# Optimization experiments

Hardware: AMD Instinct MI355X
Metric: run time of the kernel (lower is better)

Reference implementation:

```python
import jax, jax.numpy as jnp
import numpy as np

B, S, H = 4, 512, 1024
E, K, I = 8, 2, 2048

def setup_inputs() -> dict:
    key = jax.random.key(0)
    k1, k2, k3, k4, k5 = jax.random.split(key, 5)
    scale_h = 1.0 / np.sqrt(H)
    scale_i = 1.0 / np.sqrt(I)
    return {
        "hidden_states": jax.random.normal(k1, (B, S, H), dtype=jnp.float32),
        "router_w": jax.random.normal(k2, (E, H), dtype=jnp.float32) * scale_h,
        "w_gate": jax.random.normal(k3, (E, H, I), dtype=jnp.float32) * scale_h,
        "w_up": jax.random.normal(k4, (E, H, I), dtype=jnp.float32) * scale_h,
        "w_down": jax.random.normal(k5, (E, I, H), dtype=jnp.float32) * scale_i,
    }

def reference(hidden_states, router_w, w_gate, w_up, w_down):
    b, s, h = hidden_states.shape
    x = hidden_states.reshape(-1, h)              # [T, H] tokens
    T = x.shape[0]

    # ---- RouterTopK: fp32 linear -> softmax over all experts -> top-k ----
    router_logits = x.astype(jnp.float32) @ router_w.T          # [T, E]
    probs = jax.nn.softmax(router_logits, axis=-1)               # [T, E]
    top_vals, top_idx = jax.lax.top_k(probs, K)                  # [T, K]

    # normalize_top_k_affinities (norm_topk_prob=True)
    top_vals = top_vals / jnp.sum(top_vals, axis=-1, keepdims=True)

    # scatter normalized affinities into a dense [T, E] combine matrix
    aff = jnp.zeros((T, E), dtype=x.dtype).at[jnp.arange(T)[:, None], top_idx].set(top_vals.astype(x.dtype))

    # ---- ExpertMLPs: GLU (swiglu) per expert, combine weighted by affinity ----
    # Dense-per-expert computation; non-selected experts contribute 0 via aff.
    gate = jnp.einsum('th,ehi->eti', x, w_gate)                  # [E, T, I]
    up = jnp.einsum('th,ehi->eti', x, w_up)                      # [E, T, I]
    act = jax.nn.silu(gate) * up                                 # [E, T, I]
    expert_out = jnp.einsum('eti,eih->eth', act, w_down)         # [E, T, H]
    out = jnp.einsum('eth,te->th', expert_out, aff)              # [T, H]

    # _reduce_output: all-reduce over TP/world group -> identity single-device
    return out.reshape(b, s, h)
```

## Files before the change

### kernel.cpp

```cpp
#include <hip/hip_runtime.h>
#include <hip/hip_bf16.h>

#define T_TOK 2048
#define H_DIM 1024
#define E_N   8
#define I_DIM 2048

#define NT_MAX 40
#define MAX_SLOTS 5120

typedef unsigned short u16;
typedef unsigned int   u32;
typedef __bf16 bf16_t;
typedef bf16_t bf16x8 __attribute__((ext_vector_type(8)));
typedef u16    u16x8  __attribute__((ext_vector_type(8)));
typedef float  f32x4  __attribute__((ext_vector_type(4)));

#define MFMA __builtin_amdgcn_mfma_f32_16x16x32_bf16

__device__ __forceinline__ u16 bfbits(float f) {
    bf16_t b = (bf16_t)f;
    return __builtin_bit_cast(u16, b);
}

__device__ __forceinline__ void gload_lds16(const void* g, void* l) {
    __builtin_amdgcn_global_load_lds(
        (const __attribute__((address_space(1))) void*)g,
        (__attribute__((address_space(3))) void*)l, 16, 0, 0);
}

__device__ __forceinline__ int tile_off(int n, int kb) {
    return n * 64 + ((kb ^ ((n >> 1) & 7)) << 3);
}
__device__ __forceinline__ int a_off(int row, int kslot) {
    return row * 64 + ((kslot ^ (row & 7)) << 3);
}

__global__ __launch_bounds__(256) void prep_k(
    const float* __restrict__ x, const float* __restrict__ rw,
    const float* __restrict__ wg, const float* __restrict__ wu, const float* __restrict__ wd,
    u16* __restrict__ tg, u16* __restrict__ tu, u16* __restrict__ td,
    int* __restrict__ cnt, int* __restrict__ tok, float* __restrict__ wts,
    u16* __restrict__ xbf)
{
    __shared__ float S[64][132];
    int bid = blockIdx.x;

    if (bid >= 6144) {
        int wid = threadIdx.x >> 6, lane = threadIdx.x & 63;
        int t = (bid - 6144) * 4 + wid;
        const float* xr = x + (size_t)t * H_DIM;
        u16* xbr = xbf + (size_t)t * H_DIM;
        float acc[E_N];
#pragma unroll
        for (int e = 0; e < E_N; e++) acc[e] = 0.f;
        for (int j = 0; j < H_DIM / 64; j++) {
            float xv = xr[lane + 64 * j];
            xbr[lane + 64 * j] = bfbits(xv);
#pragma unroll
            for (int e = 0; e < E_N; e++)
                acc[e] += xv * rw[e * H_DIM + lane + 64 * j];
        }
#pragma unroll
        for (int e = 0; e < E_N; e++) {
            float v = acc[e];
            for (int off = 32; off; off >>= 1) v += __shfl_xor(v, off);
            acc[e] = v;
        }
        if (lane == 0) {
            int i0 = 0; float m0 = acc[0];
#pragma unroll
            for (int e = 1; e < E_N; e++) if (acc[e] > m0) { m0 = acc[e]; i0 = e; }
            int i1 = -1; float m1 = -INFINITY;
#pragma unroll
            for (int e = 0; e < E_N; e++) if (e != i0 && acc[e] > m1) { m1 = acc[e]; i1 = e; }
            float w0 = 1.f / (1.f + expf(m1 - m0));
            float w1 = 1.f - w0;
            int p0 = atomicAdd(&cnt[i0], 1);
            tok[i0 * T_TOK + p0] = t; wts[i0 * T_TOK + p0] = w0;
            int p1 = atomicAdd(&cnt[i1], 1);
            tok[i1 * T_TOK + p1] = t; wts[i1 * T_TOK + p1] = w1;
        }
        return;
    }

    int kind = bid >> 11;
    int ti = bid & 2047;
    const float* src; u16* dst; int nstr;
    if (kind < 2) {
        const float* w = kind ? wu : wg;
        int e = ti >> 8, b = ti & 15;
        int p = (ti >> 4) & 15;
        src = w + ((size_t)e * H_DIM + b * 64) * I_DIM + p * 128;
        nstr = I_DIM;
        dst = (kind ? tu : tg) + (size_t)ti * 8192;
    } else {
        int e = ti >> 8, r = ti & 255;
        int p = r >> 5, b = r & 31;
        src = wd + ((size_t)e * I_DIM + b * 64) * H_DIM + p * 128;
        nstr = H_DIM;
        dst = td + (size_t)ti * 8192;
    }
    int tid = threadIdx.x;
#pragma unroll
    for (int i = 0; i < 8; i++) {
        int idx = tid + i * 256;
        int k = idx >> 5, c4 = idx & 31;
        float4 v = *reinterpret_cast<const float4*>(src + (size_t)k * nstr + c4 * 4);
        *reinterpret_cast<float4*>(&S[k][c4 * 4]) = v;
    }
    __syncthreads();
#pragma unroll
    for (int i = 0; i < 4; i++) {
        int oidx = tid + i * 256;
        int n = oidx & 127, kb = oidx >> 7;
        u16x8 pk;
#pragma unroll
        for (int j = 0; j < 8; j++) pk[j] = bfbits(S[kb * 8 + j][n]);
        *reinterpret_cast<u16x8*>(dst + tile_off(n, kb)) = pk;
    }
}

__global__ void prefix_k(const int* __restrict__ cnt, int* __restrict__ offs_pad,
                         int* __restrict__ tile_e, int* __restrict__ tile_row0,
                         int* __restrict__ ntiles)
{
    if (threadIdx.x == 0) {
        int s = 0, nt = 0;
        for (int e = 0; e < E_N; e++) {
            offs_pad[e] = s;
            int c = cnt[e];
            int t = (c + 127) >> 7;
            for (int i = 0; i < t; i++) { tile_e[nt] = e; tile_row0[nt] = i * 128; nt++; }
            s += t * 128;
        }
        offs_pad[E_N] = s;
        *ntiles = nt;
    }
}

__global__ __launch_bounds__(512, 2) void gateup_k(
    const u16* __restrict__ xbf, const u16* __restrict__ tg, const u16* __restrict__ tu,
    const int* __restrict__ cnt, const int* __restrict__ offs_pad,
    const int* __restrict__ tile_e, const int* __restrict__ tile_row0,
    const int* __restrict__ ntiles, const int* __restrict__ tok,
    u16* __restrict__ act)
{
    int q = gridDim.x >> 3;
    int phys = blockIdx.x;
    int logical = (phys & 7) * q + (phys >> 3);
    int tb = logical % NT_MAX;
    int p  = logical / NT_MAX;
    if (tb >= *ntiles) return;
    int e = tile_e[tb], row0 = tile_row0[tb];
    int cntE = cnt[e];
    int slot0 = offs_pad[e] + row0;
    int n0 = p * 128;

    __shared__ u16 AS[2][8192], GS[2][8192], US[2][8192];

    int tid = threadIdx.x;
    int lane = tid & 63, wid = tid >> 6;
    int wm = wid & 3, wn = wid >> 2;
    int l15 = lane & 15, lg = lane >> 4;

    const u16* asrc[2];
#pragma unroll
    for (int i = 0; i < 2; i++) {
        int row = (wid * 2 + i) * 8 + (lane >> 3);
        int rc = (row0 + row < cntE) ? (row0 + row) : (cntE - 1);
        asrc[i] = xbf + (size_t)tok[e * T_TOK + rc] * H_DIM + (((lane & 7) ^ (lane >> 3)) << 3);
    }
    const u16* tgB = tg + ((size_t)(e * 16 + p) * 16) * 8192;
    const u16* tuB = tu + ((size_t)(e * 16 + p) * 16) * 8192;
    int s0 = (wid * 2) * 512;

#define STAGE_GU(bufi, t) { \
    gload_lds16(asrc[0] + (size_t)(t) * 64, &AS[bufi][s0]); \
    gload_lds16(asrc[1] + (size_t)(t) * 64, &AS[bufi][s0 + 512]); \
    gload_lds16(tgB + (size_t)(t) * 8192 + s0 + lane * 8,       &GS[bufi][s0]); \
    gload_lds16(tgB + (size_t)(t) * 8192 + s0 + 512 + lane * 8, &GS[bufi][s0 + 512]); \
    gload_lds16(tuB + (size_t)(t) * 8192 + s0 + lane * 8,       &US[bufi][s0]); \
    gload_lds16(tuB + (size_t)(t) * 8192 + s0 + 512 + lane * 8, &US[bufi][s0 + 512]); }

    f32x4 accg[2][4], accu[2][4];
#pragma unroll
    for (int a = 0; a < 2; a++)
#pragma unroll
        for (int b = 0; b < 4; b++) { accg[a][b] = (f32x4)0.f; accu[a][b] = (f32x4)0.f; }

    STAGE_GU(0, 0);

    for (int t = 0; t < 16; t++) {
        int buf = t & 1;
        if (t + 1 < 16) {
            STAGE_GU(buf ^ 1, t + 1);
            asm volatile("s_waitcnt vmcnt(6)" ::: "memory");
        } else {
            asm volatile("s_waitcnt vmcnt(0)" ::: "memory");
        }
        __builtin_amdgcn_s_barrier();
        __builtin_amdgcn_sched_barrier(0);

#pragma unroll
        for (int ks = 0; ks < 2; ks++) {
            bf16x8 af[2];
#pragma unroll
            for (int mf = 0; mf < 2; mf++) {
                int row = wm * 32 + mf * 16 + l15;
                af[mf] = *reinterpret_cast<const bf16x8*>(&AS[buf][a_off(row, ks * 4 + lg)]);
            }
            int kbr = ks * 4 + lg;
#pragma unroll
            for (int nf = 0; nf < 4; nf++) {
                int c = wn * 64 + nf * 16 + l15;
                int o = tile_off(c, kbr);
                bf16x8 bg = *reinterpret_cast<const bf16x8*>(&GS[buf][o]);
                bf16x8 bu = *reinterpret_cast<const bf16x8*>(&US[buf][o]);
#pragma unroll
                for (int mf = 0; mf < 2; mf++) {
                    accg[mf][nf] = MFMA(af[mf], bg, accg[mf][nf], 0, 0, 0);
                    accu[mf][nf] = MFMA(af[mf], bu, accu[mf][nf], 0, 0, 0);
                }
            }
        }
        __builtin_amdgcn_s_barrier();
        __builtin_amdgcn_sched_barrier(0);
    }
#undef STAGE_GU

#pragma unroll
    for (int mf = 0; mf < 2; mf++)
#pragma unroll
        for (int j = 0; j < 4; j++) {
            int rl = wm * 32 + mf * 16 + lg * 4 + j;
            bool valid = (row0 + rl) < cntE;
            size_t base = (size_t)(slot0 + rl) * I_DIM + n0;
#pragma unroll
            for (int nf = 0; nf < 4; nf++) {
                float g = accg[mf][nf][j];
                float u = accu[mf][nf][j];
                float a = valid ? (g / (1.f + expf(-g))) * u : 0.f;
                act[base + wn * 64 + nf * 16 + l15] = bfbits(a);
            }
        }
}

__global__ __launch_bounds__(512, 4) void down_k(
    const u16* __restrict__ act, const u16* __restrict__ td,
    const int* __restrict__ cnt, const int* __restrict__ offs_pad,
    const int* __restrict__ tile_e, const int* __restrict__ tile_row0,
    const int* __restrict__ ntiles, const int* __restrict__ tok,
    const float* __restrict__ wts, float* __restrict__ out)
{
    int q = gridDim.x >> 3;
    int phys = blockIdx.x;
    int logical = (phys & 7) * q + (phys >> 3);
    int tb = logical % NT_MAX;
    int rest = logical / NT_MAX;
    int p  = rest & 7;
    int kh = rest >> 3;
    if (tb >= *ntiles) return;
    int e = tile_e[tb], row0 = tile_row0[tb];
    int cntE = cnt[e];
    int slot0 = offs_pad[e] + row0;
    int h0 = p * 128;

    __shared__ u16 AS[2][8192], DS[2][8192];

    int tid = threadIdx.x;
    int lane = tid & 63, wid = tid >> 6;
    int wm = wid & 3, wn = wid >> 2;
    int l15 = lane & 15, lg = lane >> 4;

    const u16* asrc[2];
#pragma unroll
    for (int i = 0; i < 2; i++) {
        int row = (wid * 2 + i) * 8 + (lane >> 3);
        asrc[i] = act + (size_t)(slot0 + row) * I_DIM + kh * 1024
                  + (((lane & 7) ^ (lane >> 3)) << 3);
    }
    const u16* tdB = td + ((size_t)(e * 8 + p) * 32 + kh * 16) * 8192;
    int s0 = (wid * 2) * 512;

#define STAGE_D(bufi, t) { \
    gload_lds16(asrc[0] + (size_t)(t) * 64, &AS[bufi][s0]); \
    gload_lds16(asrc[1] + (size_t)(t) * 64, &AS[bufi][s0 + 512]); \
    gload_lds16(tdB + (size_t)(t) * 8192 + s0 + lane * 8,       &DS[bufi][s0]); \
    gload_lds16(tdB + (size_t)(t) * 8192 + s0 + 512 + lane * 8, &DS[bufi][s0 + 512]); }

    f32x4 acc[2][4];
#pragma unroll
    for (int a = 0; a < 2; a++)
#pragma unroll
        for (int b = 0; b < 4; b++) acc[a][b] = (f32x4)0.f;

    STAGE_D(0, 0);

    for (int t = 0; t < 16; t++) {
        int buf = t & 1;
        if (t + 1 < 16) {
            STAGE_D(buf ^ 1, t + 1);
            asm volatile("s_waitcnt vmcnt(4)" ::: "memory");
        } else {
            asm volatile("s_waitcnt vmcnt(0)" ::: "memory");
        }
        __builtin_amdgcn_s_barrier();
        __builtin_amdgcn_sched_barrier(0);

#pragma unroll
        for (int ks = 0; ks < 2; ks++) {
            bf16x8 af[2];
#pragma unroll
            for (int mf = 0; mf < 2; mf++) {
                int row = wm * 32 + mf * 16 + l15;
                af[mf] = *reinterpret_cast<const bf16x8*>(&AS[buf][a_off(row, ks * 4 + lg)]);
            }
            int kbr = ks * 4 + lg;
#pragma unroll
            for (int nf = 0; nf < 4; nf++) {
                int c = wn * 64 + nf * 16 + l15;
                bf16x8 bd = *reinterpret_cast<const bf16x8*>(&DS[buf][tile_off(c, kbr)]);
#pragma unroll
                for (int mf = 0; mf < 2; mf++)
                    acc[mf][nf] = MFMA(af[mf], bd, acc[mf][nf], 0, 0, 0);
            }
        }
        __builtin_amdgcn_s_barrier();
        __builtin_amdgcn_sched_barrier(0);
    }
#undef STAGE_D

#pragma unroll
    for (int mf = 0; mf < 2; mf++)
#pragma unroll
        for (int j = 0; j < 4; j++) {
            int rl = wm * 32 + mf * 16 + lg * 4 + j;
            int gr = row0 + rl;
            if (gr < cntE) {
                float w = wts[e * T_TOK + gr];
                int t   = tok[e * T_TOK + gr];
                size_t base = (size_t)t * H_DIM + h0;
#pragma unroll
                for (int nf = 0; nf < 4; nf++)
                    atomicAdd(&out[base + wn * 64 + nf * 16 + l15], acc[mf][nf][j] * w);
            }
        }
}

extern "C" void kernel_launch(void* const* d_in, const int* in_sizes, int n_in,
                              void* d_out, int out_size, void* d_ws, size_t ws_size,
                              hipStream_t stream)
{
    const float* x  = (const float*)d_in[0];
    const float* rw = (const float*)d_in[1];
    const float* wg = (const float*)d_in[2];
    const float* wu = (const float*)d_in[3];
    const float* wd = (const float*)d_in[4];
    float* out = (float*)d_out;

    char* ws = (char*)d_ws;
    int*   cnt       = (int*)(ws);
    int*   ntiles    = (int*)(ws + 32);
    int*   offs_pad  = (int*)(ws + 64);
    int*   tile_e    = (int*)(ws + 256);
    int*   tile_row0 = (int*)(ws + 512);
    int*   tok       = (int*)(ws + 64 * 1024);
    float* wts       = (float*)(ws + 128 * 1024);
    u16*   xbf       = (u16*)(ws + 256 * 1024);
    u16*   act       = (u16*)(ws + 4608 * 1024);

    const size_t OFF_TG = 28ull << 20;
    const size_t TSZ    = 2048ull * 16384;
    u16* tg = (u16*)(ws + OFF_TG);
    u16* tu = (u16*)(ws + OFF_TG + TSZ);
    u16* td = (u16*)(ws + OFF_TG + 2 * TSZ);

    size_t need = OFF_TG + 3 * TSZ;
    if (ws_size < need) return;

    hipMemsetAsync(cnt, 0, 32, stream);
    hipMemsetAsync(out, 0, (size_t)T_TOK * H_DIM * sizeof(float), stream);

    prep_k<<<6144 + T_TOK / 4, 256, 0, stream>>>(x, rw, wg, wu, wd, tg, tu, td,
                                                 cnt, tok, wts, xbf);
    prefix_k<<<1, 64, 0, stream>>>(cnt, offs_pad, tile_e, tile_row0, ntiles);
    gateup_k<<<NT_MAX * (I_DIM / 128), 512, 0, stream>>>(
        xbf, tg, tu, cnt, offs_pad, tile_e, tile_row0, ntiles, tok, act);
    down_k<<<NT_MAX * (H_DIM / 128) * 2, 512, 0, stream>>>(
        act, td, cnt, offs_pad, tile_e, tile_row0, ntiles, tok, wts, out);
}
```

Before: 238.7 us.

## Fuse fp32-to-bf16 weight conversion into GEMM kernels, drop prep pass

Removes the separate prep pass that converted and retiled all expert weights to bf16 in workspace. The gate/up and down GEMM kernels now read the fp32 weights directly into registers, convert them to bf16 and write swizzled tiles into LDS, with register double-buffering around the MFMA loop. This avoids writing and rereading roughly 100MB of converted weights. In exchange, each tile block re-reads fp32 weights (twice the bytes, once per token tile) using scalar strided loads instead of async global-to-LDS copies, and uses more registers.

Result: faster. 218.1 us (-8.6%).

```diff
diff --git a/kernel.cpp b/kernel.cpp
--- a/kernel.cpp
+++ b/kernel.cpp
@@ -36,88 +36,45 @@
     return row * 64 + ((kslot ^ (row & 7)) << 3);
 }
 
-__global__ __launch_bounds__(256) void prep_k(
+__global__ __launch_bounds__(256) void router_k(
     const float* __restrict__ x, const float* __restrict__ rw,
-    const float* __restrict__ wg, const float* __restrict__ wu, const float* __restrict__ wd,
-    u16* __restrict__ tg, u16* __restrict__ tu, u16* __restrict__ td,
     int* __restrict__ cnt, int* __restrict__ tok, float* __restrict__ wts,
     u16* __restrict__ xbf)
 {
-    __shared__ float S[64][132];
-    int bid = blockIdx.x;
-
-    if (bid >= 6144) {
-        int wid = threadIdx.x >> 6, lane = threadIdx.x & 63;
-        int t = (bid - 6144) * 4 + wid;
-        const float* xr = x + (size_t)t * H_DIM;
-        u16* xbr = xbf + (size_t)t * H_DIM;
-        float acc[E_N];
-#pragma unroll
-        for (int e = 0; e < E_N; e++) acc[e] = 0.f;
-        for (int j = 0; j < H_DIM / 64; j++) {
-            float xv = xr[lane + 64 * j];
-            xbr[lane + 64 * j] = bfbits(xv);
-#pragma unroll
-            for (int e = 0; e < E_N; e++)
-                acc[e] += xv * rw[e * H_DIM + lane + 64 * j];
-        }
-#pragma unroll
-        for (int e = 0; e < E_N; e++) {
-            float v = acc[e];
-            for (int off = 32; off; off >>= 1) v += __shfl_xor(v, off);
-            acc[e] = v;
-        }
-        if (lane == 0) {
-            int i0 = 0; float m0 = acc[0];
-#pragma unroll
-            for (int e = 1; e < E_N; e++) if (acc[e] > m0) { m0 = acc[e]; i0 = e; }
-            int i1 = -1; float m1 = -INFINITY;
-#pragma unroll
-            for (int e = 0; e < E_N; e++) if (e != i0 && acc[e] > m1) { m1 = acc[e]; i1 = e; }
-            float w0 = 1.f / (1.f + expf(m1 - m0));
-            float w1 = 1.f - w0;
-            int p0 = atomicAdd(&cnt[i0], 1);
-            tok[i0 * T_TOK + p0] = t; wts[i0 * T_TOK + p0] = w0;
-            int p1 = atomicAdd(&cnt[i1], 1);
-            tok[i1 * T_TOK + p1] = t; wts[i1 * T_TOK + p1] = w1;
-        }
-        return;
-    }
-
-    int kind = bid >> 11;
-    int ti = bid & 2047;
-    const float* src; u16* dst; int nstr;
-    if (kind < 2) {
-        const float* w = kind ? wu : wg;
-        int e = ti >> 8, b = ti & 15;
-        int p = (ti >> 4) & 15;
-        src = w + ((size_t)e * H_DIM + b * 64) * I_DIM + p * 128;
-        nstr = I_DIM;
-        dst = (kind ? tu : tg) + (size_t)ti * 8192;
-    } else {
-        int e = ti >> 8, r = ti & 255;
-        int p = r >> 5, b = r & 31;
-        src = wd + ((size_t)e * I_DIM + b * 64) * H_DIM + p * 128;
-        nstr = H_DIM;
-        dst = td + (size_t)ti * 8192;
-    }
-    int tid = threadIdx.x;
-#pragma unroll
-    for (int i = 0; i < 8; i++) {
-        int idx = tid + i * 256;
-        int k = idx >> 5, c4 = idx & 31;
-        float4 v = *reinterpret_cast<const float4*>(src + (size_t)k * nstr + c4 * 4);
-        *reinterpret_cast<float4*>(&S[k][c4 * 4]) = v;
-    }
-    __syncthreads();
-#pragma unroll
-    for (int i = 0; i < 4; i++) {
-        int oidx = tid + i * 256;
-        int n = oidx & 127, kb = oidx >> 7;
-        u16x8 pk;
-#pragma unroll
-        for (int j = 0; j < 8; j++) pk[j] = bfbits(S[kb * 8 + j][n]);
-        *reinterpret_cast<u16x8*>(dst + tile_off(n, kb)) = pk;
+    int wid = threadIdx.x >> 6, lane = threadIdx.x & 63;
+    int t = blockIdx.x * 4 + wid;
+    const float* xr = x + (size_t)t * H_DIM;
+    u16* xbr = xbf + (size_t)t * H_DIM;
+
+    float acc[E_N];
+#pragma unroll
+    for (int e = 0; e < E_N; e++) acc[e] = 0.f;
+    for (int j = 0; j < H_DIM / 64; j++) {
+        float xv = xr[lane + 64 * j];
+        xbr[lane + 64 * j] = bfbits(xv);
+#pragma unroll
+        for (int e = 0; e < E_N; e++)
+            acc[e] += xv * rw[e * H_DIM + lane + 64 * j];
+    }
+#pragma unroll
+    for (int e = 0; e < E_N; e++) {
+        float v = acc[e];
+        for (int off = 32; off; off >>= 1) v += __shfl_xor(v, off);
+        acc[e] = v;
+    }
+    if (lane == 0) {
+        int i0 = 0; float m0 = acc[0];
+#pragma unroll
+        for (int e = 1; e < E_N; e++) if (acc[e] > m0) { m0 = acc[e]; i0 = e; }
+        int i1 = -1; float m1 = -INFINITY;
+#pragma unroll
+        for (int e = 0; e < E_N; e++) if (e != i0 && acc[e] > m1) { m1 = acc[e]; i1 = e; }
+        float w0 = 1.f / (1.f + expf(m1 - m0));
+        float w1 = 1.f - w0;
+        int p0 = atomicAdd(&cnt[i0], 1);
+        tok[i0 * T_TOK + p0] = t; wts[i0 * T_TOK + p0] = w0;
+        int p1 = atomicAdd(&cnt[i1], 1);
+        tok[i1 * T_TOK + p1] = t; wts[i1 * T_TOK + p1] = w1;
     }
 }
 
@@ -140,7 +97,7 @@
 }
 
 __global__ __launch_bounds__(512, 2) void gateup_k(
-    const u16* __restrict__ xbf, const u16* __restrict__ tg, const u16* __restrict__ tu,
+    const u16* __restrict__ xbf, const float* __restrict__ wg, const float* __restrict__ wu,
     const int* __restrict__ cnt, const int* __restrict__ offs_pad,
     const int* __restrict__ tile_e, const int* __restrict__ tile_row0,
     const int* __restrict__ ntiles, const int* __restrict__ tok,
@@ -171,17 +128,35 @@
         int rc = (row0 + row < cntE) ? (row0 + row) : (cntE - 1);
         asrc[i] = xbf + (size_t)tok[e * T_TOK + rc] * H_DIM + (((lane & 7) ^ (lane >> 3)) << 3);
     }
-    const u16* tgB = tg + ((size_t)(e * 16 + p) * 16) * 8192;
-    const u16* tuB = tu + ((size_t)(e * 16 + p) * 16) * 8192;
     int s0 = (wid * 2) * 512;
 
-#define STAGE_GU(bufi, t) { \
-    gload_lds16(asrc[0] + (size_t)(t) * 64, &AS[bufi][s0]); \
-    gload_lds16(asrc[1] + (size_t)(t) * 64, &AS[bufi][s0 + 512]); \
-    gload_lds16(tgB + (size_t)(t) * 8192 + s0 + lane * 8,       &GS[bufi][s0]); \
-    gload_lds16(tgB + (size_t)(t) * 8192 + s0 + 512 + lane * 8, &GS[bufi][s0 + 512]); \
-    gload_lds16(tuB + (size_t)(t) * 8192 + s0 + lane * 8,       &US[bufi][s0]); \
-    gload_lds16(tuB + (size_t)(t) * 8192 + s0 + 512 + lane * 8, &US[bufi][s0 + 512]); }
+    int mat   = tid >> 8;
+    int tid8  = tid & 255;
+    int bn    = tid8 & 127;
+    int khalf = tid8 >> 7;
+    const float* wsrc = (mat ? wu : wg)
+        + ((size_t)e * H_DIM + khalf * 32) * I_DIM + n0 + bn;
+
+    float v[32];
+
+#define B_LOAD(t) { \
+    _Pragma("unroll") \
+    for (int j = 0; j < 32; j++) \
+        v[j] = wsrc[(size_t)((t) * 64 + j) * I_DIM]; }
+
+#define B_WRITE(nbuf) { \
+    u16* bdst = mat ? US[nbuf] : GS[nbuf]; \
+    _Pragma("unroll") \
+    for (int jb = 0; jb < 4; jb++) { \
+        u16x8 pk; \
+        _Pragma("unroll") \
+        for (int jj = 0; jj < 8; jj++) pk[jj] = bfbits(v[jb * 8 + jj]); \
+        *reinterpret_cast<u16x8*>(&bdst[tile_off(bn, khalf * 4 + jb)]) = pk; \
+    } }
+
+#define A_STAGE(nbuf, t) { \
+    gload_lds16(asrc[0] + (size_t)(t) * 64, &AS[nbuf][s0]); \
+    gload_lds16(asrc[1] + (size_t)(t) * 64, &AS[nbuf][s0 + 512]); }
 
     f32x4 accg[2][4], accu[2][4];
 #pragma unroll
@@ -189,17 +164,19 @@
 #pragma unroll
         for (int b = 0; b < 4; b++) { accg[a][b] = (f32x4)0.f; accu[a][b] = (f32x4)0.f; }
 
-    STAGE_GU(0, 0);
-
+    A_STAGE(0, 0);
+    B_LOAD(0);
+    B_WRITE(0);
+    __syncthreads();
+
+#pragma unroll 2
     for (int t = 0; t < 16; t++) {
         int buf = t & 1;
-        if (t + 1 < 16) {
-            STAGE_GU(buf ^ 1, t + 1);
-            asm volatile("s_waitcnt vmcnt(6)" ::: "memory");
-        } else {
-            asm volatile("s_waitcnt vmcnt(0)" ::: "memory");
-        }
-        __builtin_amdgcn_s_barrier();
+        bool more = (t + 1) < 16;
+        if (more) {
+            A_STAGE(buf ^ 1, t + 1);
+            B_LOAD(t + 1);
+        }
         __builtin_amdgcn_sched_barrier(0);
 
 #pragma unroll
@@ -224,10 +201,13 @@
                 }
             }
         }
-        __builtin_amdgcn_s_barrier();
-        __builtin_amdgcn_sched_barrier(0);
-    }
-#undef STAGE_GU
+
+        if (more) B_WRITE(buf ^ 1);
+        __syncthreads();
+    }
+#undef B_LOAD
+#undef B_WRITE
+#undef A_STAGE
 
 #pragma unroll
     for (int mf = 0; mf < 2; mf++)
@@ -247,7 +227,7 @@
 }
 
 __global__ __launch_bounds__(512, 4) void down_k(
-    const u16* __restrict__ act, const u16* __restrict__ td,
+    const u16* __restrict__ act, const float* __restrict__ wd,
     const int* __restrict__ cnt, const int* __restrict__ offs_pad,
     const int* __restrict__ tile_e, const int* __restrict__ tile_row0,
     const int* __restrict__ ntiles, const int* __restrict__ tok,
@@ -280,14 +260,31 @@
         asrc[i] = act + (size_t)(slot0 + row) * I_DIM + kh * 1024
                   + (((lane & 7) ^ (lane >> 3)) << 3);
     }
-    const u16* tdB = td + ((size_t)(e * 8 + p) * 32 + kh * 16) * 8192;
     int s0 = (wid * 2) * 512;
 
-#define STAGE_D(bufi, t) { \
-    gload_lds16(asrc[0] + (size_t)(t) * 64, &AS[bufi][s0]); \
-    gload_lds16(asrc[1] + (size_t)(t) * 64, &AS[bufi][s0 + 512]); \
-    gload_lds16(tdB + (size_t)(t) * 8192 + s0 + lane * 8,       &DS[bufi][s0]); \
-    gload_lds16(tdB + (size_t)(t) * 8192 + s0 + 512 + lane * 8, &DS[bufi][s0 + 512]); }
+    int bn = tid & 127;
+    int kq = tid >> 7;
+    const float* dsrc = wd + ((size_t)e * I_DIM + kh * 1024 + kq * 16) * H_DIM + h0 + bn;
+
+    float v[16];
+
+#define B_LOAD(t) { \
+    _Pragma("unroll") \
+    for (int j = 0; j < 16; j++) \
+        v[j] = dsrc[(size_t)((t) * 64 + j) * H_DIM]; }
+
+#define B_WRITE(nbuf) { \
+    _Pragma("unroll") \
+    for (int jb = 0; jb < 2; jb++) { \
+        u16x8 pk; \
+        _Pragma("unroll") \
+        for (int jj = 0; jj < 8; jj++) pk[jj] = bfbits(v[jb * 8 + jj]); \
+        *reinterpret_cast<u16x8*>(&DS[nbuf][tile_off(bn, kq * 2 + jb)]) = pk; \
+    } }
+
+#define A_STAGE(nbuf, t) { \
+    gload_lds16(asrc[0] + (size_t)(t) * 64, &AS[nbuf][s0]); \
+    gload_lds16(asrc[1] + (size_t)(t) * 64, &AS[nbuf][s0 + 512]); }
 
     f32x4 acc[2][4];
 #pragma unroll
@@ -295,17 +292,19 @@
 #pragma unroll
         for (int b = 0; b < 4; b++) acc[a][b] = (f32x4)0.f;
 
-    STAGE_D(0, 0);
-
+    A_STAGE(0, 0);
+    B_LOAD(0);
+    B_WRITE(0);
+    __syncthreads();
+
+#pragma unroll 2
     for (int t = 0; t < 16; t++) {
         int buf = t & 1;
-        if (t + 1 < 16) {
-            STAGE_D(buf ^ 1, t + 1);
-            asm volatile("s_waitcnt vmcnt(4)" ::: "memory");
-        } else {
-            asm volatile("s_waitcnt vmcnt(0)" ::: "memory");
-        }
-        __builtin_amdgcn_s_barrier();
+        bool more = (t + 1) < 16;
+        if (more) {
+            A_STAGE(buf ^ 1, t + 1);
+            B_LOAD(t + 1);
+        }
         __builtin_amdgcn_sched_barrier(0);
 
 #pragma unroll
@@ -326,10 +325,13 @@
                     acc[mf][nf] = MFMA(af[mf], bd, acc[mf][nf], 0, 0, 0);
             }
         }
-        __builtin_amdgcn_s_barrier();
-        __builtin_amdgcn_sched_barrier(0);
-    }
-#undef STAGE_D
+
+        if (more) B_WRITE(buf ^ 1);
+        __syncthreads();
+    }
+#undef B_LOAD
+#undef B_WRITE
+#undef A_STAGE
 
 #pragma unroll
     for (int mf = 0; mf < 2; mf++)
@@ -370,23 +372,16 @@
     u16*   xbf       = (u16*)(ws + 256 * 1024);
     u16*   act       = (u16*)(ws + 4608 * 1024);
 
-    const size_t OFF_TG = 28ull << 20;
-    const size_t TSZ    = 2048ull * 16384;
-    u16* tg = (u16*)(ws + OFF_TG);
-    u16* tu = (u16*)(ws + OFF_TG + TSZ);
-    u16* td = (u16*)(ws + OFF_TG + 2 * TSZ);
-
-    size_t need = OFF_TG + 3 * TSZ;
+    size_t need = 4608ull * 1024 + (size_t)MAX_SLOTS * I_DIM * 2;
     if (ws_size < need) return;
 
     hipMemsetAsync(cnt, 0, 32, stream);
     hipMemsetAsync(out, 0, (size_t)T_TOK * H_DIM * sizeof(float), stream);
 
-    prep_k<<<6144 + T_TOK / 4, 256, 0, stream>>>(x, rw, wg, wu, wd, tg, tu, td,
-                                                 cnt, tok, wts, xbf);
+    router_k<<<T_TOK / 4, 256, 0, stream>>>(x, rw, cnt, tok, wts, xbf);
     prefix_k<<<1, 64, 0, stream>>>(cnt, offs_pad, tile_e, tile_row0, ntiles);
     gateup_k<<<NT_MAX * (I_DIM / 128), 512, 0, stream>>>(
-        xbf, tg, tu, cnt, offs_pad, tile_e, tile_row0, ntiles, tok, act);
+        xbf, wg, wu, cnt, offs_pad, tile_e, tile_row0, ntiles, tok, act);
     down_k<<<NT_MAX * (H_DIM / 128) * 2, 512, 0, stream>>>(
-        act, td, cnt, offs_pad, tile_e, tile_row0, ntiles, tok, wts, out);
-}
+        act, wd, cnt, offs_pad, tile_e, tile_row0, ntiles, tok, wts, out);
+}
```
